# Kernel optimization log

Measured on AMD Instinct MI355X. Metric: run time of the kernel, lower is better.

Reference implementation:

```python
import jax, jax.numpy as jnp
import numpy as np

EPS = 1e-10
UNK = 2  # token id treated as OOV -> copy slot, per original (w == 2 or w >= vocab_size)


def build_sparse_selective(tokens, V):
    """tokens: [T,B] int. Returns [B,T,V+T] float32.
    Row t+1 gets a one-hot 1.0 at column tokens[t] (or 5.0 at column V+t if OOV/unk),
    everything else EPS — faithful to get_sparse_selective_input (minus vocab-dependent
    slot words, unreachable for in-range random ids)."""
    T, B = tokens.shape
    res = jnp.full((B, T, V + T), EPS, dtype=jnp.float32)
    w = tokens[:-1]                                   # [T-1, B]
    t_idx = jnp.arange(T - 1)
    is_copy = (w == UNK) | (w >= V)
    col = jnp.where(is_copy, V + t_idx[:, None], w)   # [T-1, B]
    val = jnp.where(is_copy, 5.0, 1.0).astype(jnp.float32)
    b_idx = jnp.arange(B)
    res = res.at[b_idx[None, :], (t_idx + 1)[:, None], col].set(val)
    return res


def setup_inputs() -> dict:
    key = jax.random.key(0)
    ks = jax.random.split(key, 20)
    Th, Tu, B, H, E, V = 512, 128, 8, 512, 512, 32000
    s = 1.0 / np.sqrt(H)
    inp = {
        "history_tokens": jax.random.randint(ks[0], (Th, B), 0, V, dtype=jnp.int32),
        "history_enc_out": jax.random.normal(ks[1], (Th, B, H), jnp.float32),
        "u_enc_out": jax.random.normal(ks[2], (Tu, B, H), jnp.float32),
        "c_t_input": jax.random.randint(ks[3], (1, B), 0, V, dtype=jnp.int32),
        "last_hidden": jax.random.normal(ks[4], (1, B, H), jnp.float32),
        # parameters
        "emb_W": jax.random.normal(ks[5], (V, E), jnp.float32) * 0.02,
        "attn_W": jax.random.normal(ks[6], (H, 2 * H), jnp.float32) * s,
        "attn_b": jnp.zeros((H,), jnp.float32),
        "attn_v": jax.random.normal(ks[7], (H,), jnp.float32) * s,
        "gru_Wih": jax.random.normal(ks[8], (3 * H, E + H), jnp.float32) * s,
        "gru_Whh": jax.random.normal(ks[9], (3 * H, H), jnp.float32) * s,
        "gru_bih": jnp.zeros((3 * H,), jnp.float32),
        "gru_bhh": jnp.zeros((3 * H,), jnp.float32),
        "proj_W": jax.random.normal(ks[10], (V, 2 * H), jnp.float32) * s,
        "proj_b": jnp.zeros((V,), jnp.float32),
        "copy2_W": jax.random.normal(ks[11], (H, H), jnp.float32) * s,
        "copy2_b": jnp.zeros((H,), jnp.float32),
        "pgen_W": jax.random.normal(ks[12], (1, 2 * H + E), jnp.float32) * s,
        "pgen_b": jnp.zeros((1,), jnp.float32),
    }
    return inp


def reference(history_tokens, history_enc_out, u_enc_out, c_t_input, last_hidden,
              emb_W, attn_W, attn_b, attn_v, gru_Wih, gru_Whh, gru_bih, gru_bhh,
              proj_W, proj_b, copy2_W, copy2_b, pgen_W, pgen_b):
    V = emb_W.shape[0]
    H = last_hidden.shape[-1]
    h = last_hidden[0]                                    # [B,H]
    c_embed = emb_W[c_t_input[0]]                         # [B,E]

    # --- Attn over u_enc_out ---
    enc = jnp.swapaxes(u_enc_out, 0, 1)                   # [B,Tu,H]
    Hrep = jnp.broadcast_to(h[:, None, :], enc.shape)
    energy = jnp.tanh(jnp.concatenate([Hrep, enc], -1) @ attn_W.T + attn_b)  # [B,Tu,H]
    att = jax.nn.softmax(energy @ attn_v, axis=-1)        # [B,Tu]
    context = jnp.einsum('bt,bth->bh', att, enc)          # [B,H]

    # --- single-step GRU cell (PyTorch semantics) ---
    x = jnp.concatenate([c_embed, context], -1)           # [B,E+H]
    gi = x @ gru_Wih.T + gru_bih
    gh = h @ gru_Whh.T + gru_bhh
    r = jax.nn.sigmoid(gi[:, :H] + gh[:, :H])
    z = jax.nn.sigmoid(gi[:, H:2 * H] + gh[:, H:2 * H])
    n = jnp.tanh(gi[:, 2 * H:] + r * gh[:, 2 * H:])
    h_new = (1.0 - z) * n + z * h                         # gru_out == new hidden (1 layer, 1 step)

    # --- generation score ---
    gen_score = jnp.concatenate([context, h_new], -1) @ proj_W.T + proj_b    # [B,V]

    # --- copy score through sparse selective matrix ---
    sparse = build_sparse_selective(history_tokens, V)    # [B,Th,V+Th]
    hist = jnp.swapaxes(history_enc_out, 0, 1)            # [B,Th,H]
    cs = jnp.tanh(hist @ copy2_W.T + copy2_b)             # [B,Th,H]
    score = jnp.einsum('bth,bh->bt', cs, h_new)           # [B,Th]
    m = jnp.max(score, axis=1, keepdims=True)
    e = jnp.exp(score - m)
    u_copy_score = jnp.log(jnp.einsum('bt,btv->bv', e, sparse)) + m          # [B,V+Th]

    # --- pointer-generator mixing ---
    pgen = jax.nn.sigmoid(jnp.concatenate([context, h_new, c_embed], -1) @ pgen_W.T + pgen_b)  # [B,1]
    scores = jax.nn.softmax(jnp.concatenate([gen_score * pgen, u_copy_score * (1.0 - pgen)], axis=1), axis=1)
    gen, cp = scores[:, :V], scores[:, V:]
    proba = jnp.concatenate([gen + cp[:, :V], cp[:, V:]], axis=1)            # [B,V+Th]
    return proba, h_new[None], h_new[None]
```

## Files before the change

### kernel.cpp

```cpp
#include <hip/hip_runtime.h>
#include <math.h>

#define BB 8
#define TUU 128
#define THH 512
#define HDIM 512
#define VOC 32000
#define WID_ (VOC + THH)

#define OFF_GH      0
#define OFF_BIASATT 12288
#define OFF_CEMB    16384
#define OFF_LATT    20480
#define OFF_SSUM    21504
#define OFF_SCORE   21568
#define OFF_EXTRA   25664
#define OFF_Y       285760
#define OFF_GI      293952
#define OFF_PGEN    306240
#define OFF_M       306248
#define OFF_EPS     306256
#define OFF_WSPLIT_BYTES 1225056

#define OUT_H1 260096
#define OUT_H2 264192

#define SM_SHIFT 20.0f

typedef __attribute__((ext_vector_type(8))) short short8;
typedef __attribute__((ext_vector_type(4))) float f32x4;

__device__ __forceinline__ float wave_sum(float v) {
#pragma unroll
    for (int m = 1; m < 64; m <<= 1) v += __shfl_xor(v, m, 64);
    return v;
}

__device__ __forceinline__ unsigned short f2bf(float x) {
    unsigned int u = __float_as_uint(x);
    unsigned int r = (u + 0x7fffu + ((u >> 16) & 1u)) >> 16;
    return (unsigned short)r;
}
__device__ __forceinline__ float bf2f(unsigned short h) {
    return __uint_as_float(((unsigned int)h) << 16);
}

__global__ __launch_bounds__(256) void k_cvt(
    const float* __restrict__ c2W, const float* __restrict__ attnW,
    unsigned short* __restrict__ wbase)
{
    int i = blockIdx.x * 256 + threadIdx.x;
    float x = c2W[i];
    unsigned short h = f2bf(x);
    wbase[i] = h;
    wbase[262144 + i] = f2bf(x - bf2f(h));
    int j = i >> 9, k = i & 511;
    float y = attnW[(size_t)j * 1024 + 512 + k];
    unsigned short h2 = f2bf(y);
    wbase[524288 + i] = h2;
    wbase[786432 + i] = f2bf(y - bf2f(h2));
}

__global__ __launch_bounds__(256) void k_prep(
    const float* __restrict__ attn_W, const float* __restrict__ attn_b,
    const float* __restrict__ gru_Whh, const float* __restrict__ gru_bhh,
    const float* __restrict__ emb_W, const int* __restrict__ c_t,
    const float* __restrict__ last_h, float* __restrict__ ws)
{
    int lane = threadIdx.x & 63;
    int wid  = __builtin_amdgcn_readfirstlane(blockIdx.x * 4 + (threadIdx.x >> 6));
    if (wid < 2048) {
        const float* wr;
        if (wid < 1536) wr = gru_Whh + (size_t)wid * 512;
        else            wr = attn_W + (size_t)(wid - 1536) * 1024;
        int k = lane * 8;
        float4 w0 = *reinterpret_cast<const float4*>(wr + k);
        float4 w1 = *reinterpret_cast<const float4*>(wr + k + 4);
        float acc[8];
#pragma unroll
        for (int b = 0; b < 8; ++b) {
            const float* hv = last_h + b * 512 + k;
            float4 h0 = *reinterpret_cast<const float4*>(hv);
            float4 h1 = *reinterpret_cast<const float4*>(hv + 4);
            acc[b] = w0.x*h0.x + w0.y*h0.y + w0.z*h0.z + w0.w*h0.w
                   + w1.x*h1.x + w1.y*h1.y + w1.z*h1.z + w1.w*h1.w;
        }
#pragma unroll
        for (int b = 0; b < 8; ++b) acc[b] = wave_sum(acc[b]);
        if (lane == 0) {
            if (wid < 1536) {
                float bias = gru_bhh[wid];
#pragma unroll
                for (int b = 0; b < 8; ++b) ws[OFF_GH + b * 1536 + wid] = acc[b] + bias;
            } else {
                int j = wid - 1536;
                float bias = attn_b[j];
#pragma unroll
                for (int b = 0; b < 8; ++b) ws[OFF_BIASATT + b * 512 + j] = acc[b] + bias;
            }
        }
    } else {
        int cw = wid - 2048;
        int idx = cw * 64 + lane;
        int b = idx >> 9, k = idx & 511;
        ws[OFF_CEMB + idx] = emb_W[(size_t)c_t[b] * 512 + k];
    }
}

__global__ __launch_bounds__(256) void k_mfma_tanh(
    const float* __restrict__ A,
    const unsigned short* __restrict__ Whi, const unsigned short* __restrict__ Wlo,
    const float* __restrict__ bias, int bstride,
    const float* __restrict__ wvp, int wstride,
    float* __restrict__ outp, int Mout)
{
    __shared__ short As[2][64][40];
    __shared__ short Ws[2][128][40];
    int tid  = threadIdx.x;
    int lane = tid & 63;
    int wv   = tid >> 6;
    int rbase = blockIdx.x * 64;
    int j0    = blockIdx.y * 128;

    f32x4 acc[4][2];
#pragma unroll
    for (int mt = 0; mt < 4; ++mt)
#pragma unroll
        for (int nt = 0; nt < 2; ++nt) acc[mt][nt] = (f32x4)0.0f;

    int q8  = (lane >> 4) * 8;
    int l15 = lane & 15;
    int ra  = tid >> 2, kk = (tid & 3) * 8;
    int jw  = tid >> 1, kh = (tid & 1) * 16;

    for (int kc = 0; kc < 16; ++kc) {
        int k0 = kc * 32;
        {
            const float* ap = A + (size_t)(rbase + ra) * 512 + k0 + kk;
            float4 a0 = *reinterpret_cast<const float4*>(ap);
            float4 a1 = *reinterpret_cast<const float4*>(ap + 4);
            float vals[8] = {a0.x, a0.y, a0.z, a0.w, a1.x, a1.y, a1.z, a1.w};
            union { short8 v; short s[8]; } hi, lo;
#pragma unroll
            for (int i = 0; i < 8; ++i) {
                unsigned short h = f2bf(vals[i]);
                hi.s[i] = (short)h;
                lo.s[i] = (short)f2bf(vals[i] - bf2f(h));
            }
            *reinterpret_cast<short8*>(&As[0][ra][kk]) = hi.v;
            *reinterpret_cast<short8*>(&As[1][ra][kk]) = lo.v;
        }
        {
            const short8* wph = reinterpret_cast<const short8*>(Whi + (size_t)(j0 + jw) * 512 + k0 + kh);
            const short8* wpl = reinterpret_cast<const short8*>(Wlo + (size_t)(j0 + jw) * 512 + k0 + kh);
            *reinterpret_cast<short8*>(&Ws[0][jw][kh])     = wph[0];
            *reinterpret_cast<short8*>(&Ws[0][jw][kh + 8]) = wph[1];
            *reinterpret_cast<short8*>(&Ws[1][jw][kh])     = wpl[0];
            *reinterpret_cast<short8*>(&Ws[1][jw][kh + 8]) = wpl[1];
        }
        __syncthreads();

        short8 ah[4], al[4], bh[2], bl[2];
#pragma unroll
        for (int mt = 0; mt < 4; ++mt) {
            ah[mt] = *reinterpret_cast<const short8*>(&As[0][mt * 16 + l15][q8]);
            al[mt] = *reinterpret_cast<const short8*>(&As[1][mt * 16 + l15][q8]);
        }
#pragma unroll
        for (int nt = 0; nt < 2; ++nt) {
            bh[nt] = *reinterpret_cast<const short8*>(&Ws[0][wv * 32 + nt * 16 + l15][q8]);
            bl[nt] = *reinterpret_cast<const short8*>(&Ws[1][wv * 32 + nt * 16 + l15][q8]);
        }
#pragma unroll
        for (int mt = 0; mt < 4; ++mt)
#pragma unroll
            for (int nt = 0; nt < 2; ++nt) {
                acc[mt][nt] = __builtin_amdgcn_mfma_f32_16x16x32_bf16(ah[mt], bh[nt], acc[mt][nt], 0, 0, 0);
                acc[mt][nt] = __builtin_amdgcn_mfma_f32_16x16x32_bf16(ah[mt], bl[nt], acc[mt][nt], 0, 0, 0);
                acc[mt][nt] = __builtin_amdgcn_mfma_f32_16x16x32_bf16(al[mt], bh[nt], acc[mt][nt], 0, 0, 0);
            }
        __syncthreads();
    }

    int q = lane >> 4;
#pragma unroll
    for (int mt = 0; mt < 4; ++mt) {
        float s[4];
#pragma unroll
        for (int r = 0; r < 4; ++r) {
            int row = rbase + mt * 16 + q * 4 + r;
            int b = row & 7;
            float v = 0.f;
#pragma unroll
            for (int nt = 0; nt < 2; ++nt) {
                int jj = j0 + wv * 32 + nt * 16 + l15;
                float e = acc[mt][nt][r] + bias[b * bstride + jj];
                v += tanhf(e) * wvp[b * wstride + jj];
            }
#pragma unroll
            for (int m = 1; m < 16; m <<= 1) v += __shfl_xor(v, m, 64);
            s[r] = v;
        }
        if (l15 == 0) {
#pragma unroll
            for (int r = 0; r < 4; ++r) {
                int row = rbase + mt * 16 + q * 4 + r;
                atomicAdd(outp + (row & 7) * Mout + (row >> 3), s[r]);
            }
        }
    }
}

__global__ __launch_bounds__(256) void k_attn_ctx(
    const float* __restrict__ u_enc, float* __restrict__ ws)
{
    __shared__ float red[256];
    __shared__ float att[128];
    int b = blockIdx.x, tid = threadIdx.x;
    float l = (tid < 128) ? ws[OFF_LATT + b * 128 + tid] : -1e30f;
    red[tid] = l; __syncthreads();
    for (int s = 128; s > 0; s >>= 1) {
        if (tid < s) red[tid] = fmaxf(red[tid], red[tid + s]);
        __syncthreads();
    }
    float mm = red[0]; __syncthreads();
    float e = (tid < 128) ? expf(l - mm) : 0.f;
    if (tid < 128) att[tid] = e;
    red[tid] = e; __syncthreads();
    for (int s = 128; s > 0; s >>= 1) {
        if (tid < s) red[tid] += red[tid + s];
        __syncthreads();
    }
    float S = red[0]; __syncthreads();
    float c0 = 0.f, c1 = 0.f;
    for (int t = 0; t < 128; ++t) {
        float a = att[t];
        const float* er = u_enc + (size_t)t * 4096 + b * 512;
        c0 += a * er[tid];
        c1 += a * er[tid + 256];
    }
    float inv = 1.0f / S;
    ws[OFF_Y + b * 1024 + tid]       = c0 * inv;
    ws[OFF_Y + b * 1024 + tid + 256] = c1 * inv;
}

__global__ __launch_bounds__(256) void k_gi(
    const float* __restrict__ gru_Wih, const float* __restrict__ gru_bih,
    float* __restrict__ ws)
{
    int lane = threadIdx.x & 63;
    int r = __builtin_amdgcn_readfirstlane(blockIdx.x * 4 + (threadIdx.x >> 6));
    const float* wr = gru_Wih + (size_t)r * 1024;
    float4 w[4];
#pragma unroll
    for (int p = 0; p < 4; ++p)
        w[p] = *reinterpret_cast<const float4*>(wr + lane * 4 + p * 256);
    float acc[8];
#pragma unroll
    for (int b = 0; b < 8; ++b) {
        acc[b] = 0.f;
#pragma unroll
        for (int p = 0; p < 4; ++p) {
            int k = lane * 4 + p * 256;
            const float* xs = (p < 2) ? (ws + OFF_CEMB + b * 512 + k)
                                      : (ws + OFF_Y + b * 1024 + (k - 512));
            float4 x4 = *reinterpret_cast<const float4*>(xs);
            acc[b] += w[p].x*x4.x + w[p].y*x4.y + w[p].z*x4.z + w[p].w*x4.w;
        }
    }
#pragma unroll
    for (int b = 0; b < 8; ++b) acc[b] = wave_sum(acc[b]);
    if (lane == 0) {
        float bias = gru_bih[r];
#pragma unroll
        for (int b = 0; b < 8; ++b) ws[OFF_GI + b * 1536 + r] = acc[b] + bias;
    }
}

__global__ __launch_bounds__(256) void k_gru(
    const float* __restrict__ last_h,
    const float* __restrict__ pgen_W, const float* __restrict__ pgen_b,
    float* __restrict__ ws, float* __restrict__ out)
{
    __shared__ float red[256];
    int b = blockIdx.x, tid = threadIdx.x;
    const float* gi = ws + OFF_GI + b * 1536;
    const float* gh = ws + OFF_GH + b * 1536;
    float pp = 0.f;
#pragma unroll
    for (int q = 0; q < 2; ++q) {
        int i = tid + q * 256;
        float r = 1.f / (1.f + expf(-(gi[i] + gh[i])));
        float z = 1.f / (1.f + expf(-(gi[512 + i] + gh[512 + i])));
        float n = tanhf(gi[1024 + i] + r * gh[1024 + i]);
        float h = last_h[b * 512 + i];
        float hn = (1.f - z) * n + z * h;
        ws[OFF_Y + b * 1024 + 512 + i] = hn;
        out[OUT_H1 + b * 512 + i] = hn;
        out[OUT_H2 + b * 512 + i] = hn;
        float cx = ws[OFF_Y + b * 1024 + i];
        float ce = ws[OFF_CEMB + b * 512 + i];
        pp += cx * pgen_W[i] + hn * pgen_W[512 + i] + ce * pgen_W[1024 + i];
    }
    red[tid] = pp; __syncthreads();
    for (int s = 128; s > 0; s >>= 1) {
        if (tid < s) red[tid] += red[tid + s];
        __syncthreads();
    }
    if (tid == 0) ws[OFF_PGEN + b] = 1.f / (1.f + expf(-(red[0] + pgen_b[0])));
}

__global__ __launch_bounds__(256) void k_proj(
    const float* __restrict__ projW, const float* __restrict__ projb,
    const float* __restrict__ ws, float* __restrict__ out)
{
    int lane = threadIdx.x & 63;
    int gw = blockIdx.x * 4 + (threadIdx.x >> 6);
    int nw = gridDim.x * 4;
    float4 yreg[8][4];
#pragma unroll
    for (int b = 0; b < 8; ++b)
#pragma unroll
        for (int p = 0; p < 4; ++p)
            yreg[b][p] = *reinterpret_cast<const float4*>(ws + OFF_Y + b * 1024 + p * 256 + lane * 4);

    for (int v = gw; v < VOC; v += nw) {
        const float4* wr = reinterpret_cast<const float4*>(projW + (size_t)v * 1024);
        float4 w0 = wr[lane], w1 = wr[64 + lane], w2 = wr[128 + lane], w3 = wr[192 + lane];
        float acc[8];
#pragma unroll
        for (int b = 0; b < 8; ++b) {
            acc[b] = w0.x*yreg[b][0].x + w0.y*yreg[b][0].y + w0.z*yreg[b][0].z + w0.w*yreg[b][0].w
                   + w1.x*yreg[b][1].x + w1.y*yreg[b][1].y + w1.z*yreg[b][1].z + w1.w*yreg[b][1].w
                   + w2.x*yreg[b][2].x + w2.y*yreg[b][2].y + w2.z*yreg[b][2].z + w2.w*yreg[b][2].w
                   + w3.x*yreg[b][3].x + w3.y*yreg[b][3].y + w3.z*yreg[b][3].z + w3.w*yreg[b][3].w;
        }
#pragma unroll
        for (int b = 0; b < 8; ++b) acc[b] = wave_sum(acc[b]);
        if (lane == 0) {
            float pb = projb[v];
#pragma unroll
            for (int b = 0; b < 8; ++b) out[b * WID_ + v] = acc[b] + pb;
        }
    }
}

__global__ __launch_bounds__(512) void k_copy_sm(
    const int* __restrict__ htok, float* __restrict__ ws)
{
    __shared__ float red[512];
    __shared__ float es[512];
    int b = blockIdx.x, t = threadIdx.x;
    float s = ws[OFF_SCORE + b * 512 + t];
    red[t] = s; __syncthreads();
    for (int st = 256; st > 0; st >>= 1) {
        if (t < st) red[t] = fmaxf(red[t], red[t + st]);
        __syncthreads();
    }
    float m = red[0]; __syncthreads();
    float e = expf(s - m);
    es[t] = e; red[t] = e; __syncthreads();
    for (int st = 256; st > 0; st >>= 1) {
        if (t < st) red[t] += red[t + st];
        __syncthreads();
    }
    if (t == 0) {
        ws[OFF_M + b]   = m;
        ws[OFF_EPS + b] = 1e-10f * red[0];
    }
    if (t < 511) {
        int tok = htok[t * 8 + b];
        int col = (tok == 2) ? (VOC + t) : tok;
        float val = (tok == 2) ? 5.0f : 1.0f;
        atomicAdd(ws + OFF_EXTRA + b * WID_ + col, (val - 1e-10f) * es[t + 1]);
    }
}

__global__ __launch_bounds__(256) void k_numer(
    float* __restrict__ ws, float* __restrict__ out)
{
    __shared__ float red[256];
    int b = blockIdx.x, tid = threadIdx.x;
    int start = blockIdx.y * 2032;
    float gp   = ws[OFF_PGEN + b];
    float cq   = 1.f - gp;
    float m    = ws[OFF_M + b];
    float epsS = ws[OFF_EPS + b];
    float loc = 0.f;
    for (int w = start + tid; w < start + 2032; w += 256) {
        float ex = ws[OFF_EXTRA + b * WID_ + w];
        float cv = cq * (logf(epsS + ex) + m);
        float num = expf(cv - SM_SHIFT);
        if (w < VOC) num += expf(gp * out[b * WID_ + w] - SM_SHIFT);
        out[b * WID_ + w] = num;
        loc += num;
    }
    red[tid] = loc; __syncthreads();
    for (int st = 128; st > 0; st >>= 1) {
        if (tid < st) red[tid] += red[tid + st];
        __syncthreads();
    }
    if (tid == 0) atomicAdd(ws + OFF_SSUM + b, red[0]);
}

__global__ __launch_bounds__(256) void k_scale(
    const float* __restrict__ ws, float* __restrict__ out)
{
    int b = blockIdx.x, tid = threadIdx.x;
    int start = blockIdx.y * 2032;
    float inv = 1.f / ws[OFF_SSUM + b];
    for (int w = start + tid; w < start + 2032; w += 256)
        out[b * WID_ + w] *= inv;
}

extern "C" void kernel_launch(void* const* d_in, const int* in_sizes, int n_in,
                              void* d_out, int out_size, void* d_ws, size_t ws_size,
                              hipStream_t stream)
{
    (void)in_sizes; (void)n_in; (void)out_size; (void)ws_size;
    const int*   htok  = (const int*)d_in[0];
    const float* henc  = (const float*)d_in[1];
    const float* uenc  = (const float*)d_in[2];
    const int*   ct    = (const int*)d_in[3];
    const float* lasth = (const float*)d_in[4];
    const float* embW  = (const float*)d_in[5];
    const float* attnW = (const float*)d_in[6];
    const float* attnb = (const float*)d_in[7];
    const float* attnv = (const float*)d_in[8];
    const float* gWih  = (const float*)d_in[9];
    const float* gWhh  = (const float*)d_in[10];
    const float* gbih  = (const float*)d_in[11];
    const float* gbhh  = (const float*)d_in[12];
    const float* projW = (const float*)d_in[13];
    const float* projb = (const float*)d_in[14];
    const float* c2W   = (const float*)d_in[15];
    const float* c2b   = (const float*)d_in[16];
    const float* pgW   = (const float*)d_in[17];
    const float* pgb   = (const float*)d_in[18];
    float* ws  = (float*)d_ws;
    float* out = (float*)d_out;
    unsigned short* wsplit = (unsigned short*)((char*)d_ws + OFF_WSPLIT_BYTES);

    hipMemsetAsync((char*)d_ws + (size_t)OFF_LATT * 4, 0,
                   (size_t)(OFF_Y - OFF_LATT) * 4, stream);

    k_cvt<<<1024, 256, 0, stream>>>(c2W, attnW, wsplit);
    k_prep<<<528, 256, 0, stream>>>(attnW, attnb, gWhh, gbhh, embW, ct, lasth, ws);
    k_mfma_tanh<<<dim3(16, 4), 256, 0, stream>>>(
        uenc, wsplit + 524288, wsplit + 786432,
        ws + OFF_BIASATT, 512, attnv, 0, ws + OFF_LATT, 128);
    k_attn_ctx<<<8, 256, 0, stream>>>(uenc, ws);
    k_gi<<<384, 256, 0, stream>>>(gWih, gbih, ws);
    k_gru<<<8, 256, 0, stream>>>(lasth, pgW, pgb, ws, out);
    k_mfma_tanh<<<dim3(64, 4), 256, 0, stream>>>(
        henc, wsplit, wsplit + 262144,
        c2b, 0, ws + OFF_Y + 512, 1024, ws + OFF_SCORE, 512);
    k_proj<<<500, 256, 0, stream>>>(projW, projb, ws, out);
    k_copy_sm<<<8, 512, 0, stream>>>(htok, ws);
    k_numer<<<dim3(8, 16), 256, 0, stream>>>(ws, out);
    k_scale<<<dim3(8, 16), 256, 0, stream>>>(ws, out);
}
```

Before: 359.2 us.

## Fuse kernel launches: merge prep, co-schedule copy GEMM with projection, single-pass softmax

Folds weight conversion, the recurrent/attention matvecs and embedding gather into one launch. The copy-score MFMA GEMM and the vocabulary projection now run as two block ranges of one grid, so they can overlap. The numerator and scale passes become a single kernel with one 1024-thread block per batch that keeps values in registers and normalizes in place. This cuts launch count and a round trip through the output, but the final softmax now runs on only 8 blocks, which reduces parallelism.

```diff
diff --git a/kernel.cpp b/kernel.cpp
--- a/kernel.cpp
+++ b/kernel.cpp
@@ -45,31 +45,29 @@
     return __uint_as_float(((unsigned int)h) << 16);
 }
 
-__global__ __launch_bounds__(256) void k_cvt(
-    const float* __restrict__ c2W, const float* __restrict__ attnW,
-    unsigned short* __restrict__ wbase)
-{
-    int i = blockIdx.x * 256 + threadIdx.x;
-    float x = c2W[i];
-    unsigned short h = f2bf(x);
-    wbase[i] = h;
-    wbase[262144 + i] = f2bf(x - bf2f(h));
-    int j = i >> 9, k = i & 511;
-    float y = attnW[(size_t)j * 1024 + 512 + k];
-    unsigned short h2 = f2bf(y);
-    wbase[524288 + i] = h2;
-    wbase[786432 + i] = f2bf(y - bf2f(h2));
-}
-
-__global__ __launch_bounds__(256) void k_prep(
-    const float* __restrict__ attn_W, const float* __restrict__ attn_b,
+__global__ __launch_bounds__(256) void k_pre(
+    const float* __restrict__ c2W, const float* __restrict__ attn_W,
+    const float* __restrict__ attn_b,
     const float* __restrict__ gru_Whh, const float* __restrict__ gru_bhh,
     const float* __restrict__ emb_W, const int* __restrict__ c_t,
-    const float* __restrict__ last_h, float* __restrict__ ws)
-{
-    int lane = threadIdx.x & 63;
-    int wid  = __builtin_amdgcn_readfirstlane(blockIdx.x * 4 + (threadIdx.x >> 6));
-    if (wid < 2048) {
+    const float* __restrict__ last_h,
+    unsigned short* __restrict__ wbase, float* __restrict__ ws)
+{
+    int bx = blockIdx.x, tid = threadIdx.x;
+    if (bx < 1024) {
+        int i = bx * 256 + tid;
+        float x = c2W[i];
+        unsigned short h = f2bf(x);
+        wbase[i] = h;
+        wbase[262144 + i] = f2bf(x - bf2f(h));
+        int j = i >> 9, k = i & 511;
+        float y = attn_W[(size_t)j * 1024 + 512 + k];
+        unsigned short h2 = f2bf(y);
+        wbase[524288 + i] = h2;
+        wbase[786432 + i] = f2bf(y - bf2f(h2));
+    } else if (bx < 1536) {
+        int lane = tid & 63;
+        int wid = __builtin_amdgcn_readfirstlane((bx - 1024) * 4 + (tid >> 6));
         const float* wr;
         if (wid < 1536) wr = gru_Whh + (size_t)wid * 512;
         else            wr = attn_W + (size_t)(wid - 1536) * 1024;
@@ -100,27 +98,24 @@
             }
         }
     } else {
-        int cw = wid - 2048;
-        int idx = cw * 64 + lane;
+        int idx = (bx - 1536) * 256 + tid;
         int b = idx >> 9, k = idx & 511;
         ws[OFF_CEMB + idx] = emb_W[(size_t)c_t[b] * 512 + k];
     }
 }
 
-__global__ __launch_bounds__(256) void k_mfma_tanh(
+__device__ __forceinline__ void mfma_tanh_body(
     const float* __restrict__ A,
     const unsigned short* __restrict__ Whi, const unsigned short* __restrict__ Wlo,
     const float* __restrict__ bias, int bstride,
     const float* __restrict__ wvp, int wstride,
-    float* __restrict__ outp, int Mout)
-{
-    __shared__ short As[2][64][40];
-    __shared__ short Ws[2][128][40];
+    float* __restrict__ outp, int Mout,
+    int rbase, int j0,
+    short (*As)[64][40], short (*Ws)[128][40])
+{
     int tid  = threadIdx.x;
     int lane = tid & 63;
     int wv   = tid >> 6;
-    int rbase = blockIdx.x * 64;
-    int j0    = blockIdx.y * 128;
 
     f32x4 acc[4][2];
 #pragma unroll
@@ -209,6 +204,18 @@
             }
         }
     }
+}
+
+__global__ __launch_bounds__(256) void k_attgemm(
+    const float* __restrict__ A, const unsigned short* __restrict__ wsplit,
+    const float* __restrict__ attnv, float* __restrict__ ws)
+{
+    __shared__ short As[2][64][40];
+    __shared__ short Ws[2][128][40];
+    mfma_tanh_body(A, wsplit + 524288, wsplit + 786432,
+                   ws + OFF_BIASATT, 512, attnv, 0,
+                   ws + OFF_LATT, 128,
+                   blockIdx.x * 64, blockIdx.y * 128, As, Ws);
 }
 
 __global__ __launch_bounds__(256) void k_attn_ctx(
@@ -310,37 +317,49 @@
     if (tid == 0) ws[OFF_PGEN + b] = 1.f / (1.f + expf(-(red[0] + pgen_b[0])));
 }
 
-__global__ __launch_bounds__(256) void k_proj(
+__global__ __launch_bounds__(256) void k_gemmproj(
+    const float* __restrict__ henc, const unsigned short* __restrict__ wsplit,
+    const float* __restrict__ c2b,
     const float* __restrict__ projW, const float* __restrict__ projb,
-    const float* __restrict__ ws, float* __restrict__ out)
-{
-    int lane = threadIdx.x & 63;
-    int gw = blockIdx.x * 4 + (threadIdx.x >> 6);
-    int nw = gridDim.x * 4;
-    float4 yreg[8][4];
-#pragma unroll
-    for (int b = 0; b < 8; ++b)
-#pragma unroll
-        for (int p = 0; p < 4; ++p)
-            yreg[b][p] = *reinterpret_cast<const float4*>(ws + OFF_Y + b * 1024 + p * 256 + lane * 4);
-
-    for (int v = gw; v < VOC; v += nw) {
-        const float4* wr = reinterpret_cast<const float4*>(projW + (size_t)v * 1024);
-        float4 w0 = wr[lane], w1 = wr[64 + lane], w2 = wr[128 + lane], w3 = wr[192 + lane];
-        float acc[8];
-#pragma unroll
-        for (int b = 0; b < 8; ++b) {
-            acc[b] = w0.x*yreg[b][0].x + w0.y*yreg[b][0].y + w0.z*yreg[b][0].z + w0.w*yreg[b][0].w
-                   + w1.x*yreg[b][1].x + w1.y*yreg[b][1].y + w1.z*yreg[b][1].z + w1.w*yreg[b][1].w
-                   + w2.x*yreg[b][2].x + w2.y*yreg[b][2].y + w2.z*yreg[b][2].z + w2.w*yreg[b][2].w
-                   + w3.x*yreg[b][3].x + w3.y*yreg[b][3].y + w3.z*yreg[b][3].z + w3.w*yreg[b][3].w;
-        }
-#pragma unroll
-        for (int b = 0; b < 8; ++b) acc[b] = wave_sum(acc[b]);
-        if (lane == 0) {
-            float pb = projb[v];
-#pragma unroll
-            for (int b = 0; b < 8; ++b) out[b * WID_ + v] = acc[b] + pb;
+    float* __restrict__ ws, float* __restrict__ out)
+{
+    if (blockIdx.x < 256) {
+        __shared__ short As[2][64][40];
+        __shared__ short Ws[2][128][40];
+        int rbase = (blockIdx.x >> 2) * 64;
+        int j0    = (blockIdx.x & 3) * 128;
+        mfma_tanh_body(henc, wsplit, wsplit + 262144,
+                       c2b, 0, ws + OFF_Y + 512, 1024,
+                       ws + OFF_SCORE, 512, rbase, j0, As, Ws);
+    } else {
+        int lane = threadIdx.x & 63;
+        int gw = (blockIdx.x - 256) * 4 + (threadIdx.x >> 6);
+        const int nw = 500 * 4;
+        float4 yreg[8][4];
+#pragma unroll
+        for (int b = 0; b < 8; ++b)
+#pragma unroll
+            for (int p = 0; p < 4; ++p)
+                yreg[b][p] = *reinterpret_cast<const float4*>(ws + OFF_Y + b * 1024 + p * 256 + lane * 4);
+
+        for (int v = gw; v < VOC; v += nw) {
+            const float4* wr = reinterpret_cast<const float4*>(projW + (size_t)v * 1024);
+            float4 w0 = wr[lane], w1 = wr[64 + lane], w2 = wr[128 + lane], w3 = wr[192 + lane];
+            float acc[8];
+#pragma unroll
+            for (int b = 0; b < 8; ++b) {
+                acc[b] = w0.x*yreg[b][0].x + w0.y*yreg[b][0].y + w0.z*yreg[b][0].z + w0.w*yreg[b][0].w
+                       + w1.x*yreg[b][1].x + w1.y*yreg[b][1].y + w1.z*yreg[b][1].z + w1.w*yreg[b][1].w
+                       + w2.x*yreg[b][2].x + w2.y*yreg[b][2].y + w2.z*yreg[b][2].z + w2.w*yreg[b][2].w
+                       + w3.x*yreg[b][3].x + w3.y*yreg[b][3].y + w3.z*yreg[b][3].z + w3.w*yreg[b][3].w;
+            }
+#pragma unroll
+            for (int b = 0; b < 8; ++b) acc[b] = wave_sum(acc[b]);
+            if (lane == 0) {
+                float pb = projb[v];
+#pragma unroll
+                for (int b = 0; b < 8; ++b) out[b * WID_ + v] = acc[b] + pb;
+            }
         }
     }
 }
@@ -376,41 +395,34 @@
     }
 }
 
-__global__ __launch_bounds__(256) void k_numer(
+__global__ __launch_bounds__(1024) void k_final2(
     float* __restrict__ ws, float* __restrict__ out)
 {
-    __shared__ float red[256];
+    __shared__ float red[1024];
     int b = blockIdx.x, tid = threadIdx.x;
-    int start = blockIdx.y * 2032;
     float gp   = ws[OFF_PGEN + b];
     float cq   = 1.f - gp;
     float m    = ws[OFF_M + b];
     float epsS = ws[OFF_EPS + b];
+    float nums[32];
     float loc = 0.f;
-    for (int w = start + tid; w < start + 2032; w += 256) {
+    int cnt = 0;
+    for (int w = tid; w < WID_; w += 1024, ++cnt) {
         float ex = ws[OFF_EXTRA + b * WID_ + w];
-        float cv = cq * (logf(epsS + ex) + m);
-        float num = expf(cv - SM_SHIFT);
+        float num = expf(cq * (logf(epsS + ex) + m) - SM_SHIFT);
         if (w < VOC) num += expf(gp * out[b * WID_ + w] - SM_SHIFT);
-        out[b * WID_ + w] = num;
+        nums[cnt] = num;
         loc += num;
     }
     red[tid] = loc; __syncthreads();
-    for (int st = 128; st > 0; st >>= 1) {
+    for (int st = 512; st > 0; st >>= 1) {
         if (tid < st) red[tid] += red[tid + st];
         __syncthreads();
     }
-    if (tid == 0) atomicAdd(ws + OFF_SSUM + b, red[0]);
-}
-
-__global__ __launch_bounds__(256) void k_scale(
-    const float* __restrict__ ws, float* __restrict__ out)
-{
-    int b = blockIdx.x, tid = threadIdx.x;
-    int start = blockIdx.y * 2032;
-    float inv = 1.f / ws[OFF_SSUM + b];
-    for (int w = start + tid; w < start + 2032; w += 256)
-        out[b * WID_ + w] *= inv;
+    float inv = 1.f / red[0];
+    cnt = 0;
+    for (int w = tid; w < WID_; w += 1024, ++cnt)
+        out[b * WID_ + w] = nums[cnt] * inv;
 }
 
 extern "C" void kernel_launch(void* const* d_in, const int* in_sizes, int n_in,
@@ -444,19 +456,13 @@
     hipMemsetAsync((char*)d_ws + (size_t)OFF_LATT * 4, 0,
                    (size_t)(OFF_Y - OFF_LATT) * 4, stream);
 
-    k_cvt<<<1024, 256, 0, stream>>>(c2W, attnW, wsplit);
-    k_prep<<<528, 256, 0, stream>>>(attnW, attnb, gWhh, gbhh, embW, ct, lasth, ws);
-    k_mfma_tanh<<<dim3(16, 4), 256, 0, stream>>>(
-        uenc, wsplit + 524288, wsplit + 786432,
-        ws + OFF_BIASATT, 512, attnv, 0, ws + OFF_LATT, 128);
+    k_pre<<<1552, 256, 0, stream>>>(c2W, attnW, attnb, gWhh, gbhh, embW, ct, lasth,
+                                    wsplit, ws);
+    k_attgemm<<<dim3(16, 4), 256, 0, stream>>>(uenc, wsplit, attnv, ws);
     k_attn_ctx<<<8, 256, 0, stream>>>(uenc, ws);
     k_gi<<<384, 256, 0, stream>>>(gWih, gbih, ws);
     k_gru<<<8, 256, 0, stream>>>(lasth, pgW, pgb, ws, out);
-    k_mfma_tanh<<<dim3(64, 4), 256, 0, stream>>>(
-        henc, wsplit, wsplit + 262144,
-        c2b, 0, ws + OFF_Y + 512, 1024, ws + OFF_SCORE, 512);
-    k_proj<<<500, 256, 0, stream>>>(projW, projb, ws, out);
+    k_gemmproj<<<756, 256, 0, stream>>>(henc, wsplit, c2b, projW, projb, ws, out);
     k_copy_sm<<<8, 512, 0, stream>>>(htok, ws);
-    k_numer<<<dim3(8, 16), 256, 0, stream>>>(ws, out);
-    k_scale<<<dim3(8, 16), 256, 0, stream>>>(ws, out);
-}
+    k_final2<<<8, 1024, 0, stream>>>(ws, out);
+}
```

New measurement: 366.0 us. About the same (+1.9%).
